# Kernel optimization log

Hardware: AMD Instinct MI355X
Metric: run time of the kernel (lower is better)

The kernel has to match this reference:

```python
import jax, jax.numpy as jnp
import numpy as np

N_EMBD = 1024
N_HEAD = 16
D_HEAD = N_EMBD // N_HEAD
B, T = 4, 2048


def _layernorm(x, g, b, eps=1e-5):
    mu = jnp.mean(x, axis=-1, keepdims=True)
    var = jnp.var(x, axis=-1, keepdims=True)
    return (x - mu) * jax.lax.rsqrt(var + eps) * g + b


def setup_inputs() -> dict:
    key = jax.random.key(0)
    ks = jax.random.split(key, 16)
    C = N_EMBD
    s = 0.02
    return {
        "x": jax.random.normal(ks[0], (B, T, C), jnp.float32),
        "ln1_g": jnp.ones((C,), jnp.float32),
        "ln1_b": jnp.zeros((C,), jnp.float32),
        "Wq": jax.random.normal(ks[1], (C, C), jnp.float32) * s,
        "bq": jnp.zeros((C,), jnp.float32),
        "Wk": jax.random.normal(ks[2], (C, C), jnp.float32) * s,
        "bk": jnp.zeros((C,), jnp.float32),
        "Wv": jax.random.normal(ks[3], (C, C), jnp.float32) * s,
        "bv": jnp.zeros((C,), jnp.float32),
        "Wo": jax.random.normal(ks[4], (C, C), jnp.float32) * s,
        "bo": jnp.zeros((C,), jnp.float32),
        "ln2_g": jnp.ones((C,), jnp.float32),
        "ln2_b": jnp.zeros((C,), jnp.float32),
        "W1": jax.random.normal(ks[5], (C, 4 * C), jnp.float32) * s,
        "b1": jnp.zeros((4 * C,), jnp.float32),
        "W2": jax.random.normal(ks[6], (4 * C, C), jnp.float32) * s,
        "b2": jnp.zeros((C,), jnp.float32),
    }


def reference(x, ln1_g, ln1_b, Wq, bq, Wk, bk, Wv, bv, Wo, bo,
              ln2_g, ln2_b, W1, b1, W2, b2):
    Bx, Tx, C = x.shape
    H, D = N_HEAD, D_HEAD

    # --- attention (pre-LN) ---
    h = _layernorm(x, ln1_g, ln1_b)
    q = (h @ Wq + bq).reshape(Bx, Tx, H, D)
    k = (h @ Wk + bk).reshape(Bx, Tx, H, D)
    v = (h @ Wv + bv).reshape(Bx, Tx, H, D)
    att = jnp.einsum("bqhd,bkhd->bhqk", q, k) * (1.0 / jnp.sqrt(jnp.float32(D)))
    causal = jnp.tril(jnp.ones((Tx, Tx), bool))
    att = jnp.where(causal, att, -jnp.inf)
    att = jax.nn.softmax(att, axis=-1)
    y = jnp.einsum("bhqk,bkhd->bqhd", att, v).reshape(Bx, Tx, C)
    x = x + (y @ Wo + bo)

    # --- MLP (pre-LN), exact GELU as in torch F.gelu default ---
    h2 = _layernorm(x, ln2_g, ln2_b)
    m = jax.nn.gelu(h2 @ W1 + b1, approximate=False)
    x = x + (m @ W2 + b2)
    return x
```

## Files before the change

### kernel.cpp

```cpp
#include <hip/hip_runtime.h>
#include <hip/hip_bf16.h>
#include <math.h>

#define C_EMBD 1024
#define T_SEQ  2048
#define BATCH  4
#define NHEAD  16
#define DHEAD  64

typedef __attribute__((ext_vector_type(8))) short bf16x8;
typedef __attribute__((ext_vector_type(4))) float floatx4;

#if __has_builtin(__builtin_amdgcn_exp2f)
#define EXP2F __builtin_amdgcn_exp2f
#else
#define EXP2F exp2f
#endif

static __device__ __forceinline__ floatx4 mfma16(bf16x8 a, bf16x8 b, floatx4 c) {
    return __builtin_amdgcn_mfma_f32_16x16x32_bf16(a, b, c, 0, 0, 0);
}

static __device__ __forceinline__ void gl2lds16(const void* g, void* l) {
    __builtin_amdgcn_global_load_lds(
        (const __attribute__((address_space(1))) void*)g,
        (__attribute__((address_space(3))) void*)l, 16, 0, 0);
}

__global__ __launch_bounds__(256) void transpose_cvt(
        const float* __restrict__ W, __hip_bfloat16* __restrict__ Wt, int K, int N) {
    __shared__ float tile[32][33];
    const int tid = threadIdx.x;
    const int n0 = blockIdx.x * 32, k0 = blockIdx.y * 32;
    const int r = tid >> 3, c4 = (tid & 7) * 4;
    float4 v = *(const float4*)&W[(size_t)(k0 + r) * N + n0 + c4];
    tile[r][c4 + 0] = v.x; tile[r][c4 + 1] = v.y;
    tile[r][c4 + 2] = v.z; tile[r][c4 + 3] = v.w;
    __syncthreads();
    __align__(8) __hip_bfloat16 ob[4];
    ob[0] = __float2bfloat16(tile[c4 + 0][r]);
    ob[1] = __float2bfloat16(tile[c4 + 1][r]);
    ob[2] = __float2bfloat16(tile[c4 + 2][r]);
    ob[3] = __float2bfloat16(tile[c4 + 3][r]);
    *(short4*)&Wt[(size_t)(n0 + r) * K + k0 + c4] = *(short4*)ob;
}

__global__ __launch_bounds__(256) void ln_bf16(
        const float* __restrict__ x, const float* __restrict__ g,
        const float* __restrict__ b, __hip_bfloat16* __restrict__ out) {
    const int row = blockIdx.x, tid = threadIdx.x;
    const float4 v = ((const float4*)(x + (size_t)row * C_EMBD))[tid];
    float s  = v.x + v.y + v.z + v.w;
    float sq = v.x * v.x + v.y * v.y + v.z * v.z + v.w * v.w;
    #pragma unroll
    for (int off = 1; off < 64; off <<= 1) {
        s  += __shfl_xor(s, off);
        sq += __shfl_xor(sq, off);
    }
    __shared__ float ps[4], pq[4];
    if ((tid & 63) == 0) { ps[tid >> 6] = s; pq[tid >> 6] = sq; }
    __syncthreads();
    s  = ps[0] + ps[1] + ps[2] + ps[3];
    sq = pq[0] + pq[1] + pq[2] + pq[3];
    const float mu   = s * (1.0f / C_EMBD);
    const float var  = sq * (1.0f / C_EMBD) - mu * mu;
    const float rstd = rsqrtf(var + 1e-5f);
    const float4 gv = ((const float4*)g)[tid];
    const float4 bv = ((const float4*)b)[tid];
    __align__(8) __hip_bfloat16 ob[4];
    ob[0] = __float2bfloat16((v.x - mu) * rstd * gv.x + bv.x);
    ob[1] = __float2bfloat16((v.y - mu) * rstd * gv.y + bv.y);
    ob[2] = __float2bfloat16((v.z - mu) * rstd * gv.z + bv.z);
    ob[3] = __float2bfloat16((v.w - mu) * rstd * gv.w + bv.w);
    *(short4*)&out[(size_t)row * C_EMBD + tid * 4] = *(short4*)ob;
}

template <int EP>
__global__ __launch_bounds__(256, 2) void gemm_bt(
        const __hip_bfloat16* __restrict__ A, const __hip_bfloat16* __restrict__ Bt,
        int M, int N, int K,
        const float* __restrict__ ba, const float* __restrict__ bb, const float* __restrict__ bc,
        __hip_bfloat16* __restrict__ o0, __hip_bfloat16* __restrict__ o1,
        __hip_bfloat16* __restrict__ o2, float* __restrict__ of,
        const float* __restrict__ resid) {
    __shared__ __align__(16) __hip_bfloat16 As[2][128 * 32];
    __shared__ __align__(16) __hip_bfloat16 Bs[2][128 * 32];
    const int tid  = threadIdx.x;

    const int gx  = gridDim.x;
    const int nwg = gx * gridDim.y;
    const int lin = blockIdx.x + gx * blockIdx.y;
    const int cpx = nwg >> 3;
    const int wg  = (lin & 7) * cpx + (lin >> 3);
    const int by  = (wg & 7) + 8 * (wg / (gx << 3));
    const int bx  = (wg >> 3) % gx;
    const int n0  = bx * 128;
    const int m0  = by * 128;

    const int wave = tid >> 6, lane = tid & 63;
    const int l15  = lane & 15, quad = lane >> 4;
    const int wm   = (wave & 1) * 64, wn = (wave >> 1) * 64;
    const int c0   = wave * 2;
    const int sr   = lane >> 2;
    const int sc   = (lane & 3) * 8;

    const floatx4 z4 = {0.f, 0.f, 0.f, 0.f};
    floatx4 acc[4][4];
    #pragma unroll
    for (int i = 0; i < 4; i++)
        #pragma unroll
        for (int j = 0; j < 4; j++) acc[i][j] = z4;

    auto stage = [&](const int buf, const int k0) {
        gl2lds16(&A [(m0 + c0 * 16 + sr) * K + k0 + sc],       &As[buf][c0 * 512]);
        gl2lds16(&A [(m0 + (c0 + 1) * 16 + sr) * K + k0 + sc], &As[buf][(c0 + 1) * 512]);
        gl2lds16(&Bt[(n0 + c0 * 16 + sr) * K + k0 + sc],       &Bs[buf][c0 * 512]);
        gl2lds16(&Bt[(n0 + (c0 + 1) * 16 + sr) * K + k0 + sc], &Bs[buf][(c0 + 1) * 512]);
    };

    stage(0, 0);
    const int nk = K >> 5;
    for (int t = 0; t < nk; ++t) {
        const int cur = t & 1;
        if (t + 1 < nk) {
            stage(cur ^ 1, (t + 1) * 32);
            asm volatile("s_waitcnt vmcnt(4)" ::: "memory");
        } else {
            asm volatile("s_waitcnt vmcnt(0)" ::: "memory");
        }
        __builtin_amdgcn_s_barrier();
        asm volatile("" ::: "memory");
        bf16x8 af[4], bfr[4];
        #pragma unroll
        for (int i = 0; i < 4; i++)
            af[i] = *(const bf16x8*)&As[cur][(wm + i * 16 + l15) * 32 + quad * 8];
        #pragma unroll
        for (int j = 0; j < 4; j++)
            bfr[j] = *(const bf16x8*)&Bs[cur][(wn + j * 16 + l15) * 32 + quad * 8];
        #pragma unroll
        for (int i = 0; i < 4; i++)
            #pragma unroll
            for (int j = 0; j < 4; j++)
                acc[i][j] = mfma16(af[i], bfr[j], acc[i][j]);
        asm volatile("" ::: "memory");
        __builtin_amdgcn_s_barrier();
    }

    #pragma unroll
    for (int i = 0; i < 4; i++) {
        #pragma unroll
        for (int j = 0; j < 4; j++) {
            const int col = n0 + wn + j * 16 + l15;
            #pragma unroll
            for (int r = 0; r < 4; r++) {
                const int m = m0 + wm + i * 16 + quad * 4 + r;
                float val = acc[i][j][r];
                if (EP == 0) {
                    const int which = col >> 10, cn = col & 1023;
                    const float* bp = (which == 0) ? ba : (which == 1) ? bb : bc;
                    val += bp[cn];
                    const int head = cn >> 6, d = cn & 63;
                    const int bidx = m >> 11, t = m & 2047;
                    if (which == 0) {
                        val *= 0.18033688011112042f;
                        o0[((bidx * NHEAD + head) * T_SEQ + t) * DHEAD + d] = __float2bfloat16(val);
                    } else if (which == 1) {
                        o1[((bidx * NHEAD + head) * T_SEQ + t) * DHEAD + d] = __float2bfloat16(val);
                    } else {
                        o2[((bidx * NHEAD + head) * DHEAD + d) * T_SEQ + t] = __float2bfloat16(val);
                    }
                } else if (EP == 1) {
                    val += ba[col];
                    of[m * N + col] = resid[m * N + col] + val;
                } else if (EP == 2) {
                    val += ba[col];
                    const float gl = 0.5f * val * (1.0f + erff(val * 0.70710678118654752f));
                    o0[m * N + col] = __float2bfloat16(gl);
                } else {
                    val += ba[col];
                    of[m * N + col] += val;
                }
            }
        }
    }
}

__global__ __launch_bounds__(512, 2) void gemm256_gelu(
        const __hip_bfloat16* __restrict__ A, const __hip_bfloat16* __restrict__ Bt,
        int M, int N, int K, const float* __restrict__ ba,
        __hip_bfloat16* __restrict__ o0) {
    __shared__ __align__(16) __hip_bfloat16 As[2][256 * 32];
    __shared__ __align__(16) __hip_bfloat16 Bs[2][256 * 32];
    const int tid = threadIdx.x;

    const int gx  = gridDim.x;
    const int nwg = gx * gridDim.y;
    const int lin = blockIdx.x + gx * blockIdx.y;
    const int cpx = nwg >> 3;
    const int wg  = (lin & 7) * cpx + (lin >> 3);
    const int by  = (wg & 7) + 8 * (wg / (gx << 3));
    const int bx  = (wg >> 3) % gx;
    const int n0  = bx * 256;
    const int m0  = by * 256;

    const int wave = tid >> 6, lane = tid & 63;
    const int l15  = lane & 15, quad = lane >> 4;
    const int wm   = (wave & 1) * 128;
    const int wn   = (wave >> 1) * 64;
    const int lr   = lane >> 2;
    const int gsw  = (lane & 3) ^ (lr & 3);
    const int sw   = l15 & 3;

    const floatx4 z4 = {0.f, 0.f, 0.f, 0.f};
    floatx4 acc[8][4];
    #pragma unroll
    for (int i = 0; i < 8; i++)
        #pragma unroll
        for (int j = 0; j < 4; j++) acc[i][j] = z4;

    auto stage = [&](const int buf, const int k0) {
        #pragma unroll
        for (int j = 0; j < 2; j++) {
            const int rb = wave * 32 + j * 16;
            gl2lds16(&A [(size_t)(m0 + rb + lr) * K + k0 + gsw * 8], &As[buf][rb * 32]);
            gl2lds16(&Bt[(size_t)(n0 + rb + lr) * K + k0 + gsw * 8], &Bs[buf][rb * 32]);
        }
    };

    stage(0, 0);
    const int nk = K >> 5;
    for (int t = 0; t < nk; ++t) {
        const int cur = t & 1;
        if (t + 1 < nk) {
            stage(cur ^ 1, (t + 1) * 32);
            asm volatile("s_waitcnt vmcnt(4)" ::: "memory");
        } else {
            asm volatile("s_waitcnt vmcnt(0)" ::: "memory");
        }
        __builtin_amdgcn_s_barrier();
        asm volatile("" ::: "memory");
        bf16x8 bfr[4];
        #pragma unroll
        for (int nj = 0; nj < 4; nj++)
            bfr[nj] = *(const bf16x8*)&Bs[cur][(wn + nj * 16 + l15) * 32 + ((quad ^ sw) * 8)];
        #pragma unroll
        for (int mi = 0; mi < 8; mi++) {
            const bf16x8 afa = *(const bf16x8*)&As[cur][(wm + mi * 16 + l15) * 32 + ((quad ^ sw) * 8)];
            #pragma unroll
            for (int nj = 0; nj < 4; nj++)
                acc[mi][nj] = mfma16(afa, bfr[nj], acc[mi][nj]);
        }
        asm volatile("" ::: "memory");
        __builtin_amdgcn_s_barrier();
    }

    #pragma unroll
    for (int mi = 0; mi < 8; mi++)
        #pragma unroll
        for (int nj = 0; nj < 4; nj++) {
            const int col = n0 + wn + nj * 16 + l15;
            const float bias = ba[col];
            #pragma unroll
            for (int r = 0; r < 4; r++) {
                const int m = m0 + wm + mi * 16 + quad * 4 + r;
                float val = acc[mi][nj][r] + bias;
                const float gl = 0.5f * val * (1.0f + erff(val * 0.70710678118654752f));
                o0[(size_t)m * N + col] = __float2bfloat16(gl);
            }
        }
}

__global__ __launch_bounds__(256, 2) void attn_fa(
        const __hip_bfloat16* __restrict__ q, const __hip_bfloat16* __restrict__ k,
        const __hip_bfloat16* __restrict__ vt, __hip_bfloat16* __restrict__ y) {
    __shared__ __align__(16) __hip_bfloat16 Ks[2][64 * 64];
    __shared__ __align__(16) __hip_bfloat16 Vs[2][64 * 64];
    __shared__ __align__(16) __hip_bfloat16 pl[4][32 * 72];
    const int tid = threadIdx.x;
    const int wave = tid >> 6, lane = tid & 63;
    const int l15 = lane & 15, quad = lane >> 4;
    const int sw  = l15 & 7;
    const int lr  = lane >> 3;
    const int gsw = (lane & 7) ^ lr;

    const int lin  = blockIdx.x;
    const int xcd  = lin & 7;
    const int slot = lin >> 3;
    const int bh   = xcd * 8 + (slot >> 3);
    const int jA   = slot & 7;

    const __hip_bfloat16* qp = q + (size_t)bh * T_SEQ * DHEAD;
    const __hip_bfloat16* kp = k + (size_t)bh * T_SEQ * DHEAD;
    const __hip_bfloat16* vp = vt + (size_t)bh * DHEAD * T_SEQ;
    __hip_bfloat16* myp = &pl[wave][0];
    const int b = bh >> 4, head = bh & 15;
    const floatx4 z4 = {0.f, 0.f, 0.f, 0.f};

    auto stage = [&](const int buf, const int kb) {
        #pragma unroll
        for (int j = 0; j < 2; j++) {
            const int rb = wave * 16 + j * 8;
            gl2lds16(&kp[(size_t)(kb + rb + lr) * DHEAD + gsw * 8], &Ks[buf][rb * 64]);
            gl2lds16(&vp[(size_t)(rb + lr) * T_SEQ + kb + gsw * 8], &Vs[buf][rb * 64]);
        }
    };

    auto segment = [&](const int tile) {
        const int q0 = tile * 128;
        const int qw = q0 + wave * 32;
        const int cc = tile * 2 + 1;

        bf16x8 bq[2][2];
        #pragma unroll
        for (int qi = 0; qi < 2; qi++)
            #pragma unroll
            for (int h = 0; h < 2; h++)
                bq[qi][h] = *(const bf16x8*)&qp[(qw + qi * 16 + l15) * DHEAD + h * 32 + quad * 8];

        floatx4 oac[2][4];
        #pragma unroll
        for (int qi = 0; qi < 2; qi++)
            #pragma unroll
            for (int nd = 0; nd < 4; nd++) oac[qi][nd] = z4;
        float li[2] = {0.f, 0.f};

        stage(0, 0);

        for (int t = 0; t <= cc; t++) {
            const int cur = t & 1;
            if (t < cc) {
                stage(cur ^ 1, (t + 1) * 64);
                asm volatile("s_waitcnt vmcnt(4)" ::: "memory");
            } else {
                asm volatile("s_waitcnt vmcnt(0)" ::: "memory");
            }
            __builtin_amdgcn_s_barrier();
            asm volatile("" ::: "memory");

            const int kb = t * 64;
            const bool act = (kb <= qw + 31);
            if (act) {
                const bool dg = (kb + 63 > qw);
                bf16x8 kf[4][2];
                #pragma unroll
                for (int nt = 0; nt < 4; nt++)
                    #pragma unroll
                    for (int h = 0; h < 2; h++)
                        kf[nt][h] = *(const bf16x8*)&Ks[cur][(nt * 16 + l15) * 64 + (((h * 4 + quad) ^ sw) * 8)];
                floatx4 sa[2][4];
                #pragma unroll
                for (int qi = 0; qi < 2; qi++)
                    #pragma unroll
                    for (int nt = 0; nt < 4; nt++) sa[qi][nt] = z4;
                #pragma unroll
                for (int nt = 0; nt < 4; nt++)
                    #pragma unroll
                    for (int h = 0; h < 2; h++) {
                        sa[0][nt] = mfma16(kf[nt][h], bq[0][h], sa[0][nt]);
                        sa[1][nt] = mfma16(kf[nt][h], bq[1][h], sa[1][nt]);
                    }
                if (dg) {
                    #pragma unroll
                    for (int qi = 0; qi < 2; qi++)
                        #pragma unroll
                        for (int nt = 0; nt < 4; nt++)
                            #pragma unroll
                            for (int r = 0; r < 4; r++)
                                if (kb + nt * 16 + quad * 4 + r > qw + qi * 16 + l15)
                                    sa[qi][nt][r] = -INFINITY;
                }
                #pragma unroll
                for (int qi = 0; qi < 2; qi++) {
                    float sm = 0.f;
                    #pragma unroll
                    for (int nt = 0; nt < 4; nt++) {
                        __align__(8) __hip_bfloat16 pk[4];
                        #pragma unroll
                        for (int r = 0; r < 4; r++) {
                            const float p = EXP2F(sa[qi][nt][r]);
                            sm += p;
                            pk[r] = __float2bfloat16(p);
                        }
                        *(short4*)&myp[(qi * 16 + l15) * 72 + nt * 16 + quad * 4] = *(short4*)pk;
                    }
                    li[qi] += sm;
                }
                bf16x8 vf[4][2];
                #pragma unroll
                for (int nd = 0; nd < 4; nd++)
                    #pragma unroll
                    for (int kh = 0; kh < 2; kh++)
                        vf[nd][kh] = *(const bf16x8*)&Vs[cur][(nd * 16 + l15) * 64 + (((kh * 4 + quad) ^ sw) * 8)];
                asm volatile("s_waitcnt lgkmcnt(0)" ::: "memory");
                bf16x8 pf[2][2];
                #pragma unroll
                for (int qi = 0; qi < 2; qi++)
                    #pragma unroll
                    for (int kh = 0; kh < 2; kh++)
                        pf[qi][kh] = *(const bf16x8*)&myp[(qi * 16 + l15) * 72 + kh * 32 + quad * 8];
                #pragma unroll
                for (int nd = 0; nd < 4; nd++)
                    #pragma unroll
                    for (int kh = 0; kh < 2; kh++) {
                        oac[0][nd] = mfma16(vf[nd][kh], pf[0][kh], oac[0][nd]);
                        oac[1][nd] = mfma16(vf[nd][kh], pf[1][kh], oac[1][nd]);
                    }
            }
            asm volatile("" ::: "memory");
            __builtin_amdgcn_s_barrier();
        }

        float inv[2];
        #pragma unroll
        for (int qi = 0; qi < 2; qi++) {
            float l = li[qi];
            l += __shfl_xor(l, 16);
            l += __shfl_xor(l, 32);
            inv[qi] = 1.0f / l;
        }
        #pragma unroll
        for (int qi = 0; qi < 2; qi++)
            #pragma unroll
            for (int nd = 0; nd < 4; nd++) {
                __align__(8) __hip_bfloat16 ok[4];
                #pragma unroll
                for (int r = 0; r < 4; r++) ok[r] = __float2bfloat16(oac[qi][nd][r] * inv[qi]);
                *(short4*)&myp[(qi * 16 + l15) * 72 + nd * 16 + quad * 4] = *(short4*)ok;
            }
        asm volatile("s_waitcnt lgkmcnt(0)" ::: "memory");
        #pragma unroll
        for (int half = 0; half < 2; half++) {
            const int row = half * 16 + (lane >> 2);
            const int cb  = (lane & 3) * 16;
            const bf16x8 v0 = *(const bf16x8*)&myp[row * 72 + cb];
            const bf16x8 v1 = *(const bf16x8*)&myp[row * 72 + cb + 8];
            __hip_bfloat16* yr = &y[(size_t)(b * T_SEQ + qw + row) * C_EMBD + head * DHEAD + cb];
            *(bf16x8*)yr       = v0;
            *(bf16x8*)(yr + 8) = v1;
        }
        asm volatile("s_waitcnt vmcnt(0)" ::: "memory");
    };

    segment(jA);
    segment(15 - jA);
}

extern "C" void kernel_launch(void* const* d_in, const int* in_sizes, int n_in,
                              void* d_out, int out_size, void* d_ws, size_t ws_size,
                              hipStream_t stream) {
    const float* x     = (const float*)d_in[0];
    const float* ln1_g = (const float*)d_in[1];
    const float* ln1_b = (const float*)d_in[2];
    const float* Wq    = (const float*)d_in[3];
    const float* bq    = (const float*)d_in[4];
    const float* Wk    = (const float*)d_in[5];
    const float* bk    = (const float*)d_in[6];
    const float* Wv    = (const float*)d_in[7];
    const float* bv    = (const float*)d_in[8];
    const float* Wo    = (const float*)d_in[9];
    const float* bo    = (const float*)d_in[10];
    const float* ln2_g = (const float*)d_in[11];
    const float* ln2_b = (const float*)d_in[12];
    const float* W1    = (const float*)d_in[13];
    const float* b1    = (const float*)d_in[14];
    const float* W2    = (const float*)d_in[15];
    const float* b2    = (const float*)d_in[16];
    float* out = (float*)d_out;

    char* ws = (char*)d_ws;
    __hip_bfloat16* wqkvt = (__hip_bfloat16*)(ws);
    __hip_bfloat16* wot   = (__hip_bfloat16*)(ws + 6291456);
    __hip_bfloat16* w1t   = (__hip_bfloat16*)(ws + 8388608);
    __hip_bfloat16* w2t   = (__hip_bfloat16*)(ws + 16777216);
    __hip_bfloat16* hbuf  = (__hip_bfloat16*)(ws + 25165824);
    __hip_bfloat16* qbuf  = (__hip_bfloat16*)(ws + 41943040);
    __hip_bfloat16* kbuf  = (__hip_bfloat16*)(ws + 58720256);
    __hip_bfloat16* vbuf  = (__hip_bfloat16*)(ws + 75497472);
    __hip_bfloat16* ybuf  = (__hip_bfloat16*)(ws + 92274688);
    __hip_bfloat16* mbuf  = (__hip_bfloat16*)(ws + 41943040);

    transpose_cvt<<<dim3(32, 32), 256, 0, stream>>>(Wq, wqkvt, 1024, 1024);
    transpose_cvt<<<dim3(32, 32), 256, 0, stream>>>(Wk, wqkvt + 1024 * 1024, 1024, 1024);
    transpose_cvt<<<dim3(32, 32), 256, 0, stream>>>(Wv, wqkvt + 2048 * 1024, 1024, 1024);
    transpose_cvt<<<dim3(32, 32), 256, 0, stream>>>(Wo, wot, 1024, 1024);
    transpose_cvt<<<dim3(128, 32), 256, 0, stream>>>(W1, w1t, 1024, 4096);
    transpose_cvt<<<dim3(32, 128), 256, 0, stream>>>(W2, w2t, 4096, 1024);

    ln_bf16<<<8192, 256, 0, stream>>>(x, ln1_g, ln1_b, hbuf);

    gemm_bt<0><<<dim3(24, 64), 256, 0, stream>>>(hbuf, wqkvt, 8192, 3072, 1024,
        bq, bk, bv, qbuf, kbuf, vbuf, nullptr, nullptr);

    attn_fa<<<dim3(512), 256, 0, stream>>>(qbuf, kbuf, vbuf, ybuf);

    gemm_bt<1><<<dim3(8, 64), 256, 0, stream>>>(ybuf, wot, 8192, 1024, 1024,
        bo, nullptr, nullptr, nullptr, nullptr, nullptr, out, x);

    ln_bf16<<<8192, 256, 0, stream>>>(out, ln2_g, ln2_b, hbuf);

    gemm256_gelu<<<dim3(16, 32), 512, 0, stream>>>(hbuf, w1t, 8192, 4096, 1024,
        b1, mbuf);

    gemm_bt<3><<<dim3(8, 64), 256, 0, stream>>>(mbuf, w2t, 8192, 1024, 4096,
        b2, nullptr, nullptr, nullptr, nullptr, nullptr, out, nullptr);
}
```

Baseline: 548.2 us.

## Use 8-phase pipelined 256x256 GEMM with BK=64 for QKV and FC1

Replaces the 256-tile GELU GEMM with a templated kernel that uses a K-step of 64 and splits each iteration into four phases. Each phase interleaves LDS fragment loads, a quarter of the next stages' global-to-LDS copies, barriers and priority-boosted MFMA blocks. The new kernel also takes over the QKV projection, replacing the 128-tile gemm_bt, with the head-split and transposed-V epilogue moved into it. The aim is better overlap of memory and compute and more reuse from the larger tile. The cost is twice the LDS (128KB per block) and more barriers per iteration, which may limit occupancy.

```diff
diff --git a/kernel.cpp b/kernel.cpp
--- a/kernel.cpp
+++ b/kernel.cpp
@@ -155,27 +155,9 @@
             for (int r = 0; r < 4; r++) {
                 const int m = m0 + wm + i * 16 + quad * 4 + r;
                 float val = acc[i][j][r];
-                if (EP == 0) {
-                    const int which = col >> 10, cn = col & 1023;
-                    const float* bp = (which == 0) ? ba : (which == 1) ? bb : bc;
-                    val += bp[cn];
-                    const int head = cn >> 6, d = cn & 63;
-                    const int bidx = m >> 11, t = m & 2047;
-                    if (which == 0) {
-                        val *= 0.18033688011112042f;
-                        o0[((bidx * NHEAD + head) * T_SEQ + t) * DHEAD + d] = __float2bfloat16(val);
-                    } else if (which == 1) {
-                        o1[((bidx * NHEAD + head) * T_SEQ + t) * DHEAD + d] = __float2bfloat16(val);
-                    } else {
-                        o2[((bidx * NHEAD + head) * DHEAD + d) * T_SEQ + t] = __float2bfloat16(val);
-                    }
-                } else if (EP == 1) {
+                if (EP == 1) {
                     val += ba[col];
                     of[m * N + col] = resid[m * N + col] + val;
-                } else if (EP == 2) {
-                    val += ba[col];
-                    const float gl = 0.5f * val * (1.0f + erff(val * 0.70710678118654752f));
-                    o0[m * N + col] = __float2bfloat16(gl);
                 } else {
                     val += ba[col];
                     of[m * N + col] += val;
@@ -185,12 +167,15 @@
     }
 }
 
-__global__ __launch_bounds__(512, 2) void gemm256_gelu(
+template <int EP>
+__global__ __launch_bounds__(512, 2) void gemm256_8ph(
         const __hip_bfloat16* __restrict__ A, const __hip_bfloat16* __restrict__ Bt,
-        int M, int N, int K, const float* __restrict__ ba,
-        __hip_bfloat16* __restrict__ o0) {
-    __shared__ __align__(16) __hip_bfloat16 As[2][256 * 32];
-    __shared__ __align__(16) __hip_bfloat16 Bs[2][256 * 32];
+        int M, int N, int K,
+        const float* __restrict__ ba, const float* __restrict__ bb, const float* __restrict__ bc,
+        __hip_bfloat16* __restrict__ o0, __hip_bfloat16* __restrict__ o1,
+        __hip_bfloat16* __restrict__ o2) {
+    __shared__ __align__(16) __hip_bfloat16 As[2][256 * 64];
+    __shared__ __align__(16) __hip_bfloat16 Bs[2][256 * 64];
     const int tid = threadIdx.x;
 
     const int gx  = gridDim.x;
@@ -204,12 +189,11 @@
     const int m0  = by * 256;
 
     const int wave = tid >> 6, lane = tid & 63;
-    const int l15  = lane & 15, quad = lane >> 4;
-    const int wm   = (wave & 1) * 128;
-    const int wn   = (wave >> 1) * 64;
-    const int lr   = lane >> 2;
-    const int gsw  = (lane & 3) ^ (lr & 3);
-    const int sw   = l15 & 3;
+    const int l15 = lane & 15, quad = lane >> 4;
+    const int wr  = wave >> 2, wc = wave & 3;
+    const int swz = l15 & 7;
+    const int sr8 = tid >> 3;
+    const int sg  = (tid & 7) ^ (sr8 & 7);
 
     const floatx4 z4 = {0.f, 0.f, 0.f, 0.f};
     floatx4 acc[8][4];
@@ -218,56 +202,115 @@
         #pragma unroll
         for (int j = 0; j < 4; j++) acc[i][j] = z4;
 
-    auto stage = [&](const int buf, const int k0) {
-        #pragma unroll
-        for (int j = 0; j < 2; j++) {
-            const int rb = wave * 32 + j * 16;
-            gl2lds16(&A [(size_t)(m0 + rb + lr) * K + k0 + gsw * 8], &As[buf][rb * 32]);
-            gl2lds16(&Bt[(size_t)(n0 + rb + lr) * K + k0 + gsw * 8], &Bs[buf][rb * 32]);
-        }
-    };
-
-    stage(0, 0);
-    const int nk = K >> 5;
-    for (int t = 0; t < nk; ++t) {
+    auto stA = [&](const int buf, const int half, const int k0) {
+        #pragma unroll
+        for (int s = 0; s < 2; s++) {
+            const int r0 = half * 128 + s * 64;
+            gl2lds16(&A[(size_t)(m0 + r0 + sr8) * K + k0 + sg * 8],
+                     &As[buf][r0 * 64 + wave * 512]);
+        }
+    };
+    auto stB = [&](const int buf, const int half, const int k0) {
+        #pragma unroll
+        for (int s = 0; s < 2; s++) {
+            const int r0 = half * 128 + s * 64;
+            gl2lds16(&Bt[(size_t)(n0 + r0 + sr8) * K + k0 + sg * 8],
+                     &Bs[buf][r0 * 64 + wave * 512]);
+        }
+    };
+    auto ldA = [&](const int buf, const int mi, const int ks) -> bf16x8 {
+        return *(const bf16x8*)&As[buf][(mi * 32 + wr * 16 + l15) * 64 +
+                                        (((ks * 4 + quad) ^ swz) * 8)];
+    };
+    auto ldB = [&](const int buf, const int nj, const int ks) -> bf16x8 {
+        return *(const bf16x8*)&Bs[buf][(wc * 64 + nj * 16 + l15) * 64 +
+                                        (((ks * 4 + quad) ^ swz) * 8)];
+    };
+
+    const int NT = K >> 6;
+    stA(0, 0, 0); stB(0, 0, 0); stA(0, 1, 0); stB(0, 1, 0);
+    stA(1, 0, 64); stB(1, 0, 64);
+    asm volatile("s_waitcnt vmcnt(4)" ::: "memory");
+    __builtin_amdgcn_s_barrier();
+    asm volatile("" ::: "memory");
+
+    for (int t = 0; t < NT; ++t) {
         const int cur = t & 1;
-        if (t + 1 < nk) {
-            stage(cur ^ 1, (t + 1) * 32);
-            asm volatile("s_waitcnt vmcnt(4)" ::: "memory");
-        } else {
-            asm volatile("s_waitcnt vmcnt(0)" ::: "memory");
-        }
-        __builtin_amdgcn_s_barrier();
-        asm volatile("" ::: "memory");
-        bf16x8 bfr[4];
-        #pragma unroll
-        for (int nj = 0; nj < 4; nj++)
-            bfr[nj] = *(const bf16x8*)&Bs[cur][(wn + nj * 16 + l15) * 32 + ((quad ^ sw) * 8)];
-        #pragma unroll
-        for (int mi = 0; mi < 8; mi++) {
-            const bf16x8 afa = *(const bf16x8*)&As[cur][(wm + mi * 16 + l15) * 32 + ((quad ^ sw) * 8)];
-            #pragma unroll
-            for (int nj = 0; nj < 4; nj++)
-                acc[mi][nj] = mfma16(afa, bfr[nj], acc[mi][nj]);
-        }
-        asm volatile("" ::: "memory");
-        __builtin_amdgcn_s_barrier();
+        const int kn1 = (t + 1) * 64, kn2 = (t + 2) * 64;
+        const bool s1 = (t + 1 < NT), s2 = (t + 2 < NT);
+        bf16x8 bfrag[4][2];
+        #pragma unroll
+        for (int p = 0; p < 4; ++p) {
+            bf16x8 afr[2][2];
+            if (p == 0) {
+                #pragma unroll
+                for (int nj = 0; nj < 4; nj++)
+                    #pragma unroll
+                    for (int ks = 0; ks < 2; ks++)
+                        bfrag[nj][ks] = ldB(cur, nj, ks);
+            }
+            #pragma unroll
+            for (int i = 0; i < 2; i++)
+                #pragma unroll
+                for (int ks = 0; ks < 2; ks++)
+                    afr[i][ks] = ldA(cur, 2 * p + i, ks);
+            if (p == 0)      { if (s1) stA(cur ^ 1, 1, kn1); }
+            else if (p == 1) { if (s1) stB(cur ^ 1, 1, kn1); }
+            else if (p == 2) { if (s2) stA(cur, 0, kn2); }
+            else             { if (s2) stB(cur, 0, kn2); }
+            asm volatile("" ::: "memory");
+            __builtin_amdgcn_s_barrier();
+            asm volatile("s_waitcnt lgkmcnt(0)" ::: "memory");
+            __builtin_amdgcn_s_setprio(1);
+            #pragma unroll
+            for (int i = 0; i < 2; i++)
+                #pragma unroll
+                for (int nj = 0; nj < 4; nj++)
+                    #pragma unroll
+                    for (int ks = 0; ks < 2; ks++)
+                        acc[2 * p + i][nj] = mfma16(afr[i][ks], bfrag[nj][ks], acc[2 * p + i][nj]);
+            __builtin_amdgcn_s_setprio(0);
+            if (p == 3) {
+                if (s2) { asm volatile("s_waitcnt vmcnt(4)" ::: "memory"); }
+                else    { asm volatile("s_waitcnt vmcnt(0)" ::: "memory"); }
+            }
+            asm volatile("" ::: "memory");
+            __builtin_amdgcn_s_barrier();
+            asm volatile("" ::: "memory");
+        }
     }
 
     #pragma unroll
-    for (int mi = 0; mi < 8; mi++)
+    for (int mi = 0; mi < 8; mi++) {
         #pragma unroll
         for (int nj = 0; nj < 4; nj++) {
-            const int col = n0 + wn + nj * 16 + l15;
-            const float bias = ba[col];
+            const int col = n0 + wc * 64 + nj * 16 + l15;
             #pragma unroll
             for (int r = 0; r < 4; r++) {
-                const int m = m0 + wm + mi * 16 + quad * 4 + r;
-                float val = acc[mi][nj][r] + bias;
-                const float gl = 0.5f * val * (1.0f + erff(val * 0.70710678118654752f));
-                o0[(size_t)m * N + col] = __float2bfloat16(gl);
-            }
-        }
+                const int m = m0 + mi * 32 + wr * 16 + quad * 4 + r;
+                float val = acc[mi][nj][r];
+                if (EP == 0) {
+                    const int which = col >> 10, cn = col & 1023;
+                    const float* bp = (which == 0) ? ba : (which == 1) ? bb : bc;
+                    val += bp[cn];
+                    const int head = cn >> 6, d = cn & 63;
+                    const int bidx = m >> 11, tt = m & 2047;
+                    if (which == 0) {
+                        val *= 0.18033688011112042f;
+                        o0[((bidx * NHEAD + head) * T_SEQ + tt) * DHEAD + d] = __float2bfloat16(val);
+                    } else if (which == 1) {
+                        o1[((bidx * NHEAD + head) * T_SEQ + tt) * DHEAD + d] = __float2bfloat16(val);
+                    } else {
+                        o2[((bidx * NHEAD + head) * DHEAD + d) * T_SEQ + tt] = __float2bfloat16(val);
+                    }
+                } else {
+                    val += ba[col];
+                    const float gl = 0.5f * val * (1.0f + erff(val * 0.70710678118654752f));
+                    o0[(size_t)m * N + col] = __float2bfloat16(gl);
+                }
+            }
+        }
+    }
 }
 
 __global__ __launch_bounds__(256, 2) void attn_fa(
@@ -488,8 +531,8 @@
 
     ln_bf16<<<8192, 256, 0, stream>>>(x, ln1_g, ln1_b, hbuf);
 
-    gemm_bt<0><<<dim3(24, 64), 256, 0, stream>>>(hbuf, wqkvt, 8192, 3072, 1024,
-        bq, bk, bv, qbuf, kbuf, vbuf, nullptr, nullptr);
+    gemm256_8ph<0><<<dim3(12, 32), 512, 0, stream>>>(hbuf, wqkvt, 8192, 3072, 1024,
+        bq, bk, bv, qbuf, kbuf, vbuf);
 
     attn_fa<<<dim3(512), 256, 0, stream>>>(qbuf, kbuf, vbuf, ybuf);
 
@@ -498,8 +541,8 @@
 
     ln_bf16<<<8192, 256, 0, stream>>>(out, ln2_g, ln2_b, hbuf);
 
-    gemm256_gelu<<<dim3(16, 32), 512, 0, stream>>>(hbuf, w1t, 8192, 4096, 1024,
-        b1, mbuf);
+    gemm256_8ph<2><<<dim3(16, 32), 512, 0, stream>>>(hbuf, w1t, 8192, 4096, 1024,
+        b1, nullptr, nullptr, mbuf, nullptr, nullptr);
 
     gemm_bt<3><<<dim3(8, 64), 256, 0, stream>>>(mbuf, w2t, 8192, 1024, 4096,
         b2, nullptr, nullptr, nullptr, nullptr, nullptr, out, nullptr);
```

New measurement: 544.7 us. No clear change (-0.6%).
